# Performance work log

Hardware: AMD Instinct MI355X
Metric: run time of the kernel (lower is better)

Reference implementation:

```python
import jax, jax.numpy as jnp
import numpy as np

# Module config (matches init_kwargs)
SHAPE = (32, 32)          # wire grid
KERNEL = (3, 3)           # window per dim
NUM_LAYERS = 4
NINPUTS = int(np.prod(KERNEL))        # 9
NPOS = 2 ** NINPUTS                   # 512 possible boolean input combos


def _bitmask():
    # itertools.product(range(2), repeat=NINPUTS) then transpose -> (NINPUTS, NPOS)
    # combination j, window-element m has bit (j >> (NINPUTS-1-m)) & 1
    j = jnp.arange(NPOS)
    m = jnp.arange(NINPUTS)
    return ((j[None, :] >> (NINPUTS - 1 - m)[:, None]) & 1).astype(jnp.float32)


def _convolve(x):
    # x: (B, H, W) -> (B, H, W, K) wrapped sliding windows (im2col via rolls),
    # faithful to ASIC.convolve with kernel_offset='center'.
    out = x
    for d, k in enumerate(KERNEL):
        # window element i along dim d comes from position +i (wraparound)
        out = jnp.stack([jnp.roll(out, -i, axis=1 + d) for i in range(k)], axis=out.ndim)
    out = out.reshape(x.shape + (-1,))  # (B, H, W, K) with k0 slowest-varying
    # 'center' offset: roll by prod((k-1)//2) along the LAST spatial dim (as the torch code does)
    shift = int(np.prod([(k - 1) // 2 for k in KERNEL]))
    out = jnp.roll(out, shift, axis=len(KERNEL))  # axis = last spatial axis in (B, H, W, K)
    return out


def setup_inputs() -> dict:
    key = jax.random.key(0)
    k1, k2 = jax.random.split(key)
    x = jax.random.uniform(k1, (16,) + SHAPE, dtype=jnp.float32)
    toggle_gates = jax.random.uniform(k2, (NUM_LAYERS, NPOS) + SHAPE, dtype=jnp.float32)
    return {"x": x, "toggle_gates": toggle_gates}


def reference(x, toggle_gates):
    tw = jax.nn.sigmoid(toggle_gates)       # (L, NPOS, H, W)
    bits = _bitmask()                        # (NINPUTS, NPOS)
    # embed(): shape == x spatial shape -> stride-1 slices; initial state is x, output is full state
    state = x                                # (B, H, W)
    for layer in range(NUM_LAYERS):
        conv = _convolve(state)              # (B, H, W, K)
        # soft-LUT weights: prod over window elems of (1 - |bit - input|)
        w = jnp.prod(1.0 - jnp.abs(conv[..., None] - bits), axis=-2)  # (B, H, W, NPOS)
        state = jnp.clip(jnp.einsum('bhwp,phw->bhw', w, tw[layer]), 0.0, 1.0)
    return state
```

## Files before the change

### kernel.cpp

```cpp
#include <hip/hip_runtime.h>

#define HH 32
#define WW 32
#define NPOS 512
#define TILE 8
#define PPAD 516
#define NTHR 512
#define NBLK 128
#define NLAYERS 4
#define RPAD 33
#define FSTR 16
#define FLAGV(L) (0x5EED0001 + (L))

__device__ __forceinline__ float ld_dev(const float* p) {
    return __hip_atomic_load(p, __ATOMIC_RELAXED, __HIP_MEMORY_SCOPE_AGENT);
}
__device__ __forceinline__ void st_dev(float* p, float v) {
    __hip_atomic_store(p, v, __ATOMIC_RELAXED, __HIP_MEMORY_SCOPE_AGENT);
}

__device__ __forceinline__ void neighbor_sync(int* flags, int layer, int h, int seg) {
    __syncthreads();
    const int t = threadIdx.x;
    if (t == 0) {
        __hip_atomic_store(&flags[(layer * NBLK + (h * 4 + seg)) * FSTR], FLAGV(layer),
                           __ATOMIC_RELAXED, __HIP_MEMORY_SCOPE_AGENT);
    }
    if (t < 9) {
        int dr = t / 3, ds = t % 3 - 1;
        int pid = (((h + dr) & 31) << 2) | ((seg + ds) & 3);
        const int* f = &flags[(layer * NBLK + pid) * FSTR];
        while (__hip_atomic_load(f, __ATOMIC_RELAXED, __HIP_MEMORY_SCOPE_AGENT) != FLAGV(layer)) {
            __builtin_amdgcn_s_sleep(2);
        }
    }
    __syncthreads();
}

__device__ __forceinline__ void make_v(const float c[9], float* v) {
    float a2[2], a4[4], a8[8], a16[16];
    a2[0] = 1.0f - c[4]; a2[1] = c[4];
    #pragma unroll
    for (int i = 0; i < 2; ++i)  { a4[2*i]  = a2[i]  * (1.0f - c[5]); a4[2*i+1]  = a2[i]  * c[5]; }
    #pragma unroll
    for (int i = 0; i < 4; ++i)  { a8[2*i]  = a4[i]  * (1.0f - c[6]); a8[2*i+1]  = a4[i]  * c[6]; }
    #pragma unroll
    for (int i = 0; i < 8; ++i)  { a16[2*i] = a8[i]  * (1.0f - c[7]); a16[2*i+1] = a8[i]  * c[7]; }
    #pragma unroll
    for (int i = 0; i < 16; ++i) { v[2*i]   = a16[i] * (1.0f - c[8]); v[2*i+1]   = a16[i] * c[8]; }
}

__device__ __forceinline__ float sigm(float g) {
    return __builtin_amdgcn_rcpf(1.0f + __expf(-g));
}

__global__ __launch_bounds__(NTHR) void asic_fused(
    const float* __restrict__ x,
    const float* __restrict__ tg,
    float* __restrict__ bufA,
    float* __restrict__ bufB,
    float* __restrict__ bufC,
    float* __restrict__ out,
    int* __restrict__ flags)
{
    __shared__ float  lut[NLAYERS][TILE * PPAD];
    __shared__ float2 red[2][8 * RPAD];

    const int t   = threadIdx.x;
    const int bid = blockIdx.x;
    const int h   = bid & 31;
    const int seg = bid >> 5;
    const int w0  = seg * TILE;
    const int hw0 = h * 32 + w0;

    const int th    = t & 255;
    const int bhalf = t >> 8;
    const int hwl   = th & 7;
    const int bp    = (th >> 3) & 3;
    const int oct   = th >> 5;
    const int w     = w0 + hwl;
    const int b0    = bhalf * 8 + 2 * bp;
    const int bit0 = (oct >> 2) & 1, bit1 = (oct >> 1) & 1, bit2 = oct & 1;

    #pragma unroll
    for (int k = 0; k < 2; ++k) {
        int f    = t + NTHR * k;
        int p    = f >> 1;
        int half = f & 1;
        float4 g4 = *(const float4*)(tg + p * (HH * WW) + hw0 + half * 4);
        int pb = half * 4;
        lut[0][(pb + 0) * PPAD + p] = sigm(g4.x);
        lut[0][(pb + 1) * PPAD + p] = sigm(g4.y);
        lut[0][(pb + 2) * PPAD + p] = sigm(g4.z);
        lut[0][(pb + 3) * PPAD + p] = sigm(g4.w);
    }

    float c0[9], c1[9];
    {
        const float* s0 = x + b0 * (HH * WW);
        const float* s1 = s0 + (HH * WW);
        #pragma unroll
        for (int i = 0; i < 3; ++i) {
            int row = ((h + i) & 31) * 32;
            #pragma unroll
            for (int j = 0; j < 3; ++j) {
                int idx = row + ((w + j - 1 + 32) & 31);
                c0[3 * i + j] = s0[idx];
                c1[3 * i + j] = s1[idx];
            }
        }
    }

    __syncthreads();

    #pragma unroll
    for (int k = 0; k < 6; ++k) {
        int f     = t + NTHR * k;
        int layer = 1 + (f >> 10);
        int r     = f & 1023;
        int p     = r >> 1;
        int half  = r & 1;
        float4 g4 = *(const float4*)(tg + (size_t)layer * NPOS * HH * WW + p * (HH * WW) + hw0 + half * 4);
        int pb = half * 4;
        lut[layer][(pb + 0) * PPAD + p] = sigm(g4.x);
        lut[layer][(pb + 1) * PPAD + p] = sigm(g4.y);
        lut[layer][(pb + 2) * PPAD + p] = sigm(g4.z);
        lut[layer][(pb + 3) * PPAD + p] = sigm(g4.w);
    }

    float* dsts[NLAYERS] = {bufA, bufB, bufC, out};
    const float* src = x;

    for (int layer = 0; layer < NLAYERS; ++layer) {
        float* dst = dsts[layer];

        if (layer > 0) {
            const float* s0 = src + b0 * (HH * WW);
            const float* s1 = s0 + (HH * WW);
            #pragma unroll
            for (int i = 0; i < 3; ++i) {
                int row = ((h + i) & 31) * 32;
                #pragma unroll
                for (int j = 0; j < 3; ++j) {
                    int idx = row + ((w + j - 1 + 32) & 31);
                    c0[3 * i + j] = ld_dev(s0 + idx);
                    c1[3 * i + j] = ld_dev(s1 + idx);
                }
            }
        }

        float v0[32], v1[32];
        make_v(c0, v0);
        make_v(c1, v1);

        float base0 = (bit0 ? c0[0] : 1.0f - c0[0]) * (bit1 ? c0[1] : 1.0f - c0[1]) * (bit2 ? c0[2] : 1.0f - c0[2]);
        float base1 = (bit0 ? c1[0] : 1.0f - c1[0]) * (bit1 ? c1[1] : 1.0f - c1[1]) * (bit2 ? c1[2] : 1.0f - c1[2]);
        float uA0 = base0 * (1.0f - c0[3]), uB0 = base0 * c0[3];
        float uA1 = base1 * (1.0f - c1[3]), uB1 = base1 * c1[3];

        const float4* lutp = (const float4*)(&lut[layer][0] + hwl * PPAD);
        const float4* A = lutp + (2 * oct) * 8;
        const float4* B = A + 8;
        float sA0 = 0.f, sA1 = 0.f, sB0 = 0.f, sB1 = 0.f;
        #pragma unroll
        for (int l4 = 0; l4 < 8; ++l4) {
            float4 LA = A[l4];
            float4 LB = B[l4];
            sA0 = fmaf(LA.x, v0[4*l4+0], sA0); sA0 = fmaf(LA.y, v0[4*l4+1], sA0);
            sA0 = fmaf(LA.z, v0[4*l4+2], sA0); sA0 = fmaf(LA.w, v0[4*l4+3], sA0);
            sA1 = fmaf(LA.x, v1[4*l4+0], sA1); sA1 = fmaf(LA.y, v1[4*l4+1], sA1);
            sA1 = fmaf(LA.z, v1[4*l4+2], sA1); sA1 = fmaf(LA.w, v1[4*l4+3], sA1);
            sB0 = fmaf(LB.x, v0[4*l4+0], sB0); sB0 = fmaf(LB.y, v0[4*l4+1], sB0);
            sB0 = fmaf(LB.z, v0[4*l4+2], sB0); sB0 = fmaf(LB.w, v0[4*l4+3], sB0);
            sB1 = fmaf(LB.x, v1[4*l4+0], sB1); sB1 = fmaf(LB.y, v1[4*l4+1], sB1);
            sB1 = fmaf(LB.z, v1[4*l4+2], sB1); sB1 = fmaf(LB.w, v1[4*l4+3], sB1);
        }
        float acc0 = fmaf(uA0, sA0, uB0 * sB0);
        float acc1 = fmaf(uA1, sA1, uB1 * sB1);

        red[bhalf][oct * RPAD + bp * 8 + hwl] = make_float2(acc0, acc1);
        __syncthreads();

        if (th < 64) {
            int hw  = th & 7;
            int bl  = th >> 3;
            int bpi = bl >> 1, par = bl & 1;
            float s = 0.0f;
            #pragma unroll
            for (int o = 0; o < 8; ++o) {
                float2 r = red[bhalf][o * RPAD + bpi * 8 + hw];
                s += par ? r.y : r.x;
            }
            s = fminf(fmaxf(s, 0.0f), 1.0f);
            st_dev(dst + (size_t)(bhalf * 8 + bl) * (HH * WW) + h * 32 + w0 + hw, s);
        }

        if (layer < NLAYERS - 1) neighbor_sync(flags, layer, h, seg);
        src = dst;
    }
}

extern "C" void kernel_launch(void* const* d_in, const int* in_sizes, int n_in,
                              void* d_out, int out_size, void* d_ws, size_t ws_size,
                              hipStream_t stream) {
    const float* x  = (const float*)d_in[0];
    const float* tg = (const float*)d_in[1];
    float* out  = (float*)d_out;
    float* bufA = (float*)d_ws;
    float* bufB = bufA + 16 * HH * WW;
    float* bufC = bufB + 16 * HH * WW;
    int*   flags = (int*)((char*)d_ws + 256 * 1024);

    asic_fused<<<NBLK, NTHR, 0, stream>>>(x, tg, bufA, bufB, bufC, out, flags);
}
```

Before: 70.76 us.

## Replace block barriers with wave-level shuffle reduction and per-wave neighbor flags

Threads are remapped so that each 64-lane wavefront owns two batch images for eight positions across all eight LUT octants. The cross-octant reduction now uses xor shuffles instead of a shared-memory buffer plus __syncthreads. The block-wide neighbor barrier is replaced by per-wavefront flags: each wave publishes after its stores and waits only on the matching waves of the nine neighboring blocks. It also loads all four layers' sigmoid LUTs before the first barrier, aiming to cut intra-block and inter-layer synchronization stalls, at the cost of more flag traffic and weaker, fence-based memory ordering.

```diff
diff --git a/kernel.cpp b/kernel.cpp
--- a/kernel.cpp
+++ b/kernel.cpp
@@ -8,7 +8,6 @@
 #define NTHR 512
 #define NBLK 128
 #define NLAYERS 4
-#define RPAD 33
 #define FSTR 16
 #define FLAGV(L) (0x5EED0001 + (L))
 
@@ -18,23 +17,8 @@
 __device__ __forceinline__ void st_dev(float* p, float v) {
     __hip_atomic_store(p, v, __ATOMIC_RELAXED, __HIP_MEMORY_SCOPE_AGENT);
 }
-
-__device__ __forceinline__ void neighbor_sync(int* flags, int layer, int h, int seg) {
-    __syncthreads();
-    const int t = threadIdx.x;
-    if (t == 0) {
-        __hip_atomic_store(&flags[(layer * NBLK + (h * 4 + seg)) * FSTR], FLAGV(layer),
-                           __ATOMIC_RELAXED, __HIP_MEMORY_SCOPE_AGENT);
-    }
-    if (t < 9) {
-        int dr = t / 3, ds = t % 3 - 1;
-        int pid = (((h + dr) & 31) << 2) | ((seg + ds) & 3);
-        const int* f = &flags[(layer * NBLK + pid) * FSTR];
-        while (__hip_atomic_load(f, __ATOMIC_RELAXED, __HIP_MEMORY_SCOPE_AGENT) != FLAGV(layer)) {
-            __builtin_amdgcn_s_sleep(2);
-        }
-    }
-    __syncthreads();
+__device__ __forceinline__ float sigm(float g) {
+    return __builtin_amdgcn_rcpf(1.0f + __expf(-g));
 }
 
 __device__ __forceinline__ void make_v(const float c[9], float* v) {
@@ -50,10 +34,6 @@
     for (int i = 0; i < 16; ++i) { v[2*i]   = a16[i] * (1.0f - c[8]); v[2*i+1]   = a16[i] * c[8]; }
 }
 
-__device__ __forceinline__ float sigm(float g) {
-    return __builtin_amdgcn_rcpf(1.0f + __expf(-g));
-}
-
 __global__ __launch_bounds__(NTHR) void asic_fused(
     const float* __restrict__ x,
     const float* __restrict__ tg,
@@ -63,8 +43,7 @@
     float* __restrict__ out,
     int* __restrict__ flags)
 {
-    __shared__ float  lut[NLAYERS][TILE * PPAD];
-    __shared__ float2 red[2][8 * RPAD];
+    __shared__ float lut[NLAYERS][TILE * PPAD];
 
     const int t   = threadIdx.x;
     const int bid = blockIdx.x;
@@ -72,27 +51,31 @@
     const int seg = bid >> 5;
     const int w0  = seg * TILE;
     const int hw0 = h * 32 + w0;
+    const int tid = (h << 2) | seg;
 
-    const int th    = t & 255;
-    const int bhalf = t >> 8;
-    const int hwl   = th & 7;
-    const int bp    = (th >> 3) & 3;
-    const int oct   = th >> 5;
-    const int w     = w0 + hwl;
-    const int b0    = bhalf * 8 + 2 * bp;
+    const int lane = t & 63;
+    const int wv   = t >> 6;
+    const int hwl  = lane & 7;
+    const int oct  = lane >> 3;
+    const int bh   = wv >> 2;
+    const int bp   = wv & 3;
+    const int b0   = bh * 8 + 2 * bp;
+    const int w    = w0 + hwl;
     const int bit0 = (oct >> 2) & 1, bit1 = (oct >> 1) & 1, bit2 = oct & 1;
 
     #pragma unroll
-    for (int k = 0; k < 2; ++k) {
-        int f    = t + NTHR * k;
-        int p    = f >> 1;
-        int half = f & 1;
-        float4 g4 = *(const float4*)(tg + p * (HH * WW) + hw0 + half * 4);
+    for (int k = 0; k < 8; ++k) {
+        int f     = t + NTHR * k;
+        int layer = f >> 10;
+        int r     = f & 1023;
+        int p     = r >> 1;
+        int half  = r & 1;
+        float4 g4 = *(const float4*)(tg + (size_t)layer * NPOS * HH * WW + p * (HH * WW) + hw0 + half * 4);
         int pb = half * 4;
-        lut[0][(pb + 0) * PPAD + p] = sigm(g4.x);
-        lut[0][(pb + 1) * PPAD + p] = sigm(g4.y);
-        lut[0][(pb + 2) * PPAD + p] = sigm(g4.z);
-        lut[0][(pb + 3) * PPAD + p] = sigm(g4.w);
+        lut[layer][(pb + 0) * PPAD + p] = sigm(g4.x);
+        lut[layer][(pb + 1) * PPAD + p] = sigm(g4.y);
+        lut[layer][(pb + 2) * PPAD + p] = sigm(g4.z);
+        lut[layer][(pb + 3) * PPAD + p] = sigm(g4.w);
     }
 
     float c0[9], c1[9];
@@ -113,29 +96,22 @@
 
     __syncthreads();
 
-    #pragma unroll
-    for (int k = 0; k < 6; ++k) {
-        int f     = t + NTHR * k;
-        int layer = 1 + (f >> 10);
-        int r     = f & 1023;
-        int p     = r >> 1;
-        int half  = r & 1;
-        float4 g4 = *(const float4*)(tg + (size_t)layer * NPOS * HH * WW + p * (HH * WW) + hw0 + half * 4);
-        int pb = half * 4;
-        lut[layer][(pb + 0) * PPAD + p] = sigm(g4.x);
-        lut[layer][(pb + 1) * PPAD + p] = sigm(g4.y);
-        lut[layer][(pb + 2) * PPAD + p] = sigm(g4.z);
-        lut[layer][(pb + 3) * PPAD + p] = sigm(g4.w);
-    }
-
     float* dsts[NLAYERS] = {bufA, bufB, bufC, out};
-    const float* src = x;
 
     for (int layer = 0; layer < NLAYERS; ++layer) {
         float* dst = dsts[layer];
 
         if (layer > 0) {
-            const float* s0 = src + b0 * (HH * WW);
+            if (lane < 9) {
+                int dr = lane / 3, ds = lane % 3 - 1;
+                int pid = (((h + dr) & 31) << 2) | ((seg + ds) & 3);
+                const int* f = &flags[(((layer - 1) * 8 + wv) * NBLK + pid) * FSTR];
+                while (__hip_atomic_load(f, __ATOMIC_RELAXED, __HIP_MEMORY_SCOPE_AGENT) != FLAGV(layer - 1)) {
+                    __builtin_amdgcn_s_sleep(2);
+                }
+            }
+            __atomic_signal_fence(__ATOMIC_ACQUIRE);
+            const float* s0 = dsts[layer - 1] + b0 * (HH * WW);
             const float* s1 = s0 + (HH * WW);
             #pragma unroll
             for (int i = 0; i < 3; ++i) {
@@ -178,25 +154,28 @@
         float acc0 = fmaf(uA0, sA0, uB0 * sB0);
         float acc1 = fmaf(uA1, sA1, uB1 * sB1);
 
-        red[bhalf][oct * RPAD + bp * 8 + hwl] = make_float2(acc0, acc1);
-        __syncthreads();
-
-        if (th < 64) {
-            int hw  = th & 7;
-            int bl  = th >> 3;
-            int bpi = bl >> 1, par = bl & 1;
-            float s = 0.0f;
-            #pragma unroll
-            for (int o = 0; o < 8; ++o) {
-                float2 r = red[bhalf][o * RPAD + bpi * 8 + hw];
-                s += par ? r.y : r.x;
-            }
-            s = fminf(fmaxf(s, 0.0f), 1.0f);
-            st_dev(dst + (size_t)(bhalf * 8 + bl) * (HH * WW) + h * 32 + w0 + hw, s);
+        #pragma unroll
+        for (int m = 8; m <= 32; m <<= 1) {
+            acc0 += __shfl_xor(acc0, m, 64);
+            acc1 += __shfl_xor(acc1, m, 64);
         }
 
-        if (layer < NLAYERS - 1) neighbor_sync(flags, layer, h, seg);
-        src = dst;
+        if (oct == 0) {
+            float r0 = fminf(fmaxf(acc0, 0.0f), 1.0f);
+            float r1 = fminf(fmaxf(acc1, 0.0f), 1.0f);
+            st_dev(dst + (size_t)b0 * (HH * WW) + h * 32 + w0 + hwl, r0);
+            st_dev(dst + (size_t)(b0 + 1) * (HH * WW) + h * 32 + w0 + hwl, r1);
+        }
+
+        if (layer < NLAYERS - 1) {
+            __atomic_signal_fence(__ATOMIC_RELEASE);
+            __builtin_amdgcn_s_waitcnt(0);
+            __atomic_signal_fence(__ATOMIC_RELEASE);
+            if (lane == 0) {
+                __hip_atomic_store(&flags[((layer * 8 + wv) * NBLK + tid) * FSTR], FLAGV(layer),
+                                   __ATOMIC_RELAXED, __HIP_MEMORY_SCOPE_AGENT);
+            }
+        }
     }
 }
 
```

After: 74.99 us. +6.0%, slower.
